# Performance work log

Measured on AMD Instinct MI355X. Metric: run time of the kernel, lower is better.

## Reference

```python
import jax, jax.numpy as jnp
import numpy as np

B_, L_, DM, DS, DC, EX = 4, 2048, 1024, 16, 4, 2
DI = DM * EX

def setup_inputs() -> dict:
    key = jax.random.key(0)
    ks = jax.random.split(key, 8)
    s = lambda i, shape, scale: jax.random.normal(ks[i], shape, jnp.float32) * scale
    return dict(
        x=s(0, (B_, L_, DM), 1.0),
        in_proj_w=s(1, (2 * DI, DM), 0.02),
        conv_weight=s(2, (DI, DC), 0.1),
        conv_bias=jnp.zeros((DI,), jnp.float32),
        A_log=jax.random.uniform(ks[3], (DS,), jnp.float32, -4.0, -1.0),
        D=jnp.ones((DI,), jnp.float32),
        delta_w=s(4, (DS, DI), 0.02),
        delta_b=jnp.ones((DS,), jnp.float32),
        B_w=s(5, (DS, DI), 0.02),
        C_w=s(6, (DS, DI), 0.02),
        out_proj_w=s(7, (DM, DI), 0.02),
    )

def reference(x, in_proj_w, conv_weight, conv_bias, A_log, D, delta_w, delta_b, B_w, C_w, out_proj_w):
    Bb, L, Dm = x.shape
    di, dc = conv_weight.shape
    # 1. input projection and split into ssm / gate branches
    x_inner = x @ in_proj_w.T                       # [B,L,2*di]
    x_ssm, x_gate = x_inner[..., :di], x_inner[..., di:]
    # 2. causal depthwise conv1d + SiLU (kernel size dc, per-channel weights)
    xp = jnp.pad(x_ssm, ((0, 0), (dc - 1, 0), (0, 0)))
    xc = conv_bias + sum(xp[:, k:k + L, :] * conv_weight[:, k] for k in range(dc))
    x_conv = jax.nn.silu(xc)                         # [B,L,di]
    # 3. content-aware discretization
    delta = jax.nn.softplus(x_conv @ delta_w.T + delta_b)  # [B,L,N]
    Bs = x_conv @ B_w.T                              # [B,L,N]
    Cs = x_conv @ C_w.T                              # [B,L,N]
    A = -jnp.exp(A_log)                              # [N]
    xavg = x_conv.mean(axis=-1)                      # [B,L]
    # 4. selective SSM scan over L with state h:[B,N]
    def step(h, inp):
        dt, bt, ct, xa = inp                         # [B,N],[B,N],[B,N],[B]
        h = jnp.exp(dt * A) * h + dt * bt * xa[:, None]
        return h, (h * ct).sum(-1)                   # y_t: [B]
    h0 = jnp.zeros((Bb, A.shape[0]), x.dtype)
    _, ys = jax.lax.scan(
        step, h0,
        (delta.transpose(1, 0, 2), Bs.transpose(1, 0, 2), Cs.transpose(1, 0, 2), xavg.T))
    y_ssm = ys.T[..., None]                          # [B,L,1] (broadcasts over di)
    # 5. gate, skip, output projection
    y_gated = y_ssm * jax.nn.silu(x_gate)
    y_skip = y_gated + x_conv * D
    return y_skip @ out_proj_w.T                     # [B,L,D]
```

## Files before the change

### kernel.cpp

```cpp
#include <hip/hip_runtime.h>
#include <cmath>

#define LL 2048
#define NROW 8192
#define DMODEL 1024
#define DINNER 2048
#define NSTATE 16
#define NSEG 64
#define SEGLEN 32

typedef unsigned short u16;
typedef __attribute__((ext_vector_type(8))) unsigned short u16x8;
typedef __attribute__((ext_vector_type(8))) short short8;
typedef __attribute__((ext_vector_type(4))) float floatx4;
typedef __attribute__((ext_vector_type(16))) float floatx16;

__device__ __forceinline__ float bf2f(u16 h) {
    unsigned u = ((unsigned)h) << 16;
    float f;
    __builtin_memcpy(&f, &u, 4);
    return f;
}
__device__ __forceinline__ u16 f2bf(float f) {
    unsigned u;
    __builtin_memcpy(&u, &f, 4);
    u = u + 0x7fffu + ((u >> 16) & 1u);
    return (u16)(u >> 16);
}
__device__ __forceinline__ float silu_f(float x) { return x / (1.f + __expf(-x)); }

__global__ __launch_bounds__(256) void cvt_multi(
    const float* __restrict__ s0, const float* __restrict__ s1,
    const float* __restrict__ s2, const float* __restrict__ s3,
    const float* __restrict__ s4, const float* __restrict__ s5,
    u16* __restrict__ d0, u16* __restrict__ d1, u16* __restrict__ d2,
    u16* __restrict__ d3, u16* __restrict__ d4, u16* __restrict__ d5) {
    int bid = blockIdx.x;
    const float* s;
    u16* d;
    size_t off;
    if (bid < 4096)      { s = s0; d = d0; off = (size_t)bid * 2048; }
    else if (bid < 6144) { s = s1; d = d1; off = (size_t)(bid - 4096) * 2048; }
    else if (bid < 7168) { s = s2; d = d2; off = (size_t)(bid - 6144) * 2048; }
    else if (bid < 7184) { s = s3; d = d3; off = (size_t)(bid - 7168) * 2048; }
    else if (bid < 7200) { s = s4; d = d4; off = (size_t)(bid - 7184) * 2048; }
    else                 { s = s5; d = d5; off = (size_t)(bid - 7200) * 2048; }
    size_t i = off + (size_t)threadIdx.x * 8;
    float4 a = *(const float4*)&s[i];
    float4 b = *(const float4*)&s[i + 4];
    u16x8 o;
    o[0] = f2bf(a.x); o[1] = f2bf(a.y); o[2] = f2bf(a.z); o[3] = f2bf(a.w);
    o[4] = f2bf(b.x); o[5] = f2bf(b.y); o[6] = f2bf(b.z); o[7] = f2bf(b.w);
    *(u16x8*)&d[i] = o;
}

template <int OUT_BF16>
__global__ __launch_bounds__(256) void gemm_bt_mfma(
    const u16* __restrict__ A, const u16* __restrict__ B,
    void* __restrict__ Cout, int N, int K) {
    __shared__ u16 As[128 * 32];
    __shared__ u16 Bs[128 * 32];
    const int tid = threadIdx.x;
    const int lane = tid & 63;
    const int wave = tid >> 6;
    const int bm = blockIdx.y * 128;
    const int bn = blockIdx.x * 128;

    const int kbg = (lane & 3) ^ ((lane >> 3) & 3);
    const int srow = lane >> 2;
    const u16* ag[2];
    const u16* bg[2];
#pragma unroll
    for (int p = 0; p < 2; ++p) {
        int c = wave * 2 + p;
        ag[p] = A + (size_t)(bm + c * 16 + srow) * K + kbg * 8;
        bg[p] = B + (size_t)(bn + c * 16 + srow) * K + kbg * 8;
    }
    const int frow = lane & 31;
    const int khi = lane >> 5;
    const int wr = (wave >> 1) * 64;
    const int wc = (wave & 1) * 64;
    int aoff[2][2], boff[2][2];
#pragma unroll
    for (int mi = 0; mi < 2; ++mi)
#pragma unroll
        for (int kh = 0; kh < 2; ++kh) {
            int rA = wr + mi * 32 + frow;
            int rB = wc + mi * 32 + frow;
            int kb = kh * 2 + khi;
            aoff[mi][kh] = rA * 32 + (kb ^ ((rA >> 1) & 3)) * 8;
            boff[mi][kh] = rB * 32 + (kb ^ ((rB >> 1) & 3)) * 8;
        }
    floatx16 acc[2][2];
#pragma unroll
    for (int i = 0; i < 2; ++i)
#pragma unroll
        for (int j = 0; j < 2; ++j) acc[i][j] = (floatx16)(0.f);

    for (int k0 = 0; k0 < K; k0 += 32) {
        __syncthreads();
#pragma unroll
        for (int p = 0; p < 2; ++p) {
            int c = wave * 2 + p;
            __builtin_amdgcn_global_load_lds(
                (const __attribute__((address_space(1))) void*)ag[p],
                (__attribute__((address_space(3))) void*)&As[c * 512], 16, 0, 0);
            __builtin_amdgcn_global_load_lds(
                (const __attribute__((address_space(1))) void*)bg[p],
                (__attribute__((address_space(3))) void*)&Bs[c * 512], 16, 0, 0);
            ag[p] += 32;
            bg[p] += 32;
        }
        __syncthreads();
        short8 af[2][2], bf[2][2];
#pragma unroll
        for (int mi = 0; mi < 2; ++mi)
#pragma unroll
            for (int kh = 0; kh < 2; ++kh) {
                af[mi][kh] = *(const short8*)&As[aoff[mi][kh]];
                bf[mi][kh] = *(const short8*)&Bs[boff[mi][kh]];
            }
#pragma unroll
        for (int kh = 0; kh < 2; ++kh)
#pragma unroll
            for (int mi = 0; mi < 2; ++mi)
#pragma unroll
                for (int ni = 0; ni < 2; ++ni)
                    acc[mi][ni] = __builtin_amdgcn_mfma_f32_32x32x16_bf16(
                        af[mi][kh], bf[ni][kh], acc[mi][ni], 0, 0, 0);
    }
    const int cc = lane & 31;
    const int rbase = 4 * (lane >> 5);
#pragma unroll
    for (int mi = 0; mi < 2; ++mi)
#pragma unroll
        for (int ni = 0; ni < 2; ++ni)
#pragma unroll
            for (int r = 0; r < 16; ++r) {
                int grow = bm + wr + mi * 32 + (r & 3) + 8 * (r >> 2) + rbase;
                int gcol = bn + wc + ni * 32 + cc;
                float v = acc[mi][ni][r];
                if (OUT_BF16)
                    ((u16*)Cout)[(size_t)grow * N + gcol] = f2bf(v);
                else
                    ((float*)Cout)[(size_t)grow * N + gcol] = v;
            }
}

__global__ __launch_bounds__(256) void conv_silu_avg(
    const u16* __restrict__ xin, const float* __restrict__ cw,
    const float* __restrict__ cb, u16* __restrict__ xconv,
    float* __restrict__ xavg) {
    const int blk = blockIdx.x;
    const int b = blk >> 7;
    const int lc = blk & 127;
    const int row0 = b * LL + lc * 16;
    const int tid = threadIdx.x;
    const int lane = tid & 63, wave = tid >> 6;
    const int d0 = tid * 8;
    float4 cwv[8];
    float cbv[8];
#pragma unroll
    for (int e = 0; e < 8; ++e) cwv[e] = *(const float4*)&cw[(d0 + e) * 4];
#pragma unroll
    for (int e = 0; e < 8; e += 4) {
        float4 c = *(const float4*)&cb[d0 + e];
        cbv[e] = c.x; cbv[e + 1] = c.y; cbv[e + 2] = c.z; cbv[e + 3] = c.w;
    }
    u16x8 w0, w1, w2;
    if (lc == 0) {
        w0 = (u16x8)0; w1 = (u16x8)0; w2 = (u16x8)0;
    } else {
        w0 = *(const u16x8*)&xin[(size_t)(row0 - 3) * (2 * DINNER) + d0];
        w1 = *(const u16x8*)&xin[(size_t)(row0 - 2) * (2 * DINNER) + d0];
        w2 = *(const u16x8*)&xin[(size_t)(row0 - 1) * (2 * DINNER) + d0];
    }
    float sums[16];
#pragma unroll
    for (int t = 0; t < 16; ++t) {
        u16x8 cur = *(const u16x8*)&xin[(size_t)(row0 + t) * (2 * DINNER) + d0];
        float lsum = 0.f;
        u16x8 o;
#pragma unroll
        for (int e = 0; e < 8; ++e) {
            float acc = cbv[e];
            acc += bf2f(w0[e]) * cwv[e].x;
            acc += bf2f(w1[e]) * cwv[e].y;
            acc += bf2f(w2[e]) * cwv[e].z;
            acc += bf2f(cur[e]) * cwv[e].w;
            float s = silu_f(acc);
            lsum += s;
            o[e] = f2bf(s);
        }
        *(u16x8*)&xconv[(size_t)(row0 + t) * DINNER + d0] = o;
        sums[t] = lsum;
        w0 = w1; w1 = w2; w2 = cur;
    }
#pragma unroll
    for (int off = 32; off; off >>= 1)
#pragma unroll
        for (int t = 0; t < 16; ++t) sums[t] += __shfl_down(sums[t], off);
    __shared__ float wred[4][16];
    if (lane == 0) {
#pragma unroll
        for (int t = 0; t < 16; ++t) wred[wave][t] = sums[t];
    }
    __syncthreads();
    if (tid < 16)
        xavg[row0 + tid] = (wred[0][tid] + wred[1][tid] + wred[2][tid] + wred[3][tid]) *
                           (1.f / DINNER);
}

__global__ __launch_bounds__(256) void dbc_mfma(
    const u16* __restrict__ xconv, const u16* __restrict__ wcat,
    const float* __restrict__ db, const float* __restrict__ A_log,
    const float* __restrict__ xavg,
    float* __restrict__ a_out, float* __restrict__ u_out, float* __restrict__ c_out) {
    __shared__ u16 As[128 * 32];
    __shared__ u16 Bs[48 * 32];
    const int tid = threadIdx.x;
    const int lane = tid & 63;
    const int wave = tid >> 6;
    const int bm = blockIdx.x * 128;

    const int kbg = (lane & 3) ^ ((lane >> 3) & 3);
    const int srow = lane >> 2;
    const u16* ag[2];
#pragma unroll
    for (int p = 0; p < 2; ++p) {
        int c = wave * 2 + p;
        ag[p] = xconv + (size_t)(bm + c * 16 + srow) * DINNER + kbg * 8;
    }
    const u16* bgp = wcat + (size_t)(wave * 16 + srow) * DINNER + kbg * 8;
    const int fr = lane & 15;
    const int kb = lane >> 4;
    const int kbs = kb ^ ((fr >> 1) & 3);
    int aoff[2], boff[3];
#pragma unroll
    for (int mi = 0; mi < 2; ++mi) aoff[mi] = (wave * 32 + mi * 16 + fr) * 32 + kbs * 8;
#pragma unroll
    for (int ni = 0; ni < 3; ++ni) boff[ni] = (ni * 16 + fr) * 32 + kbs * 8;

    floatx4 acc[2][3];
#pragma unroll
    for (int mi = 0; mi < 2; ++mi)
#pragma unroll
        for (int ni = 0; ni < 3; ++ni) acc[mi][ni] = (floatx4){0.f, 0.f, 0.f, 0.f};

    for (int k0 = 0; k0 < DINNER; k0 += 32) {
        __syncthreads();
#pragma unroll
        for (int p = 0; p < 2; ++p) {
            int c = wave * 2 + p;
            __builtin_amdgcn_global_load_lds(
                (const __attribute__((address_space(1))) void*)ag[p],
                (__attribute__((address_space(3))) void*)&As[c * 512], 16, 0, 0);
            ag[p] += 32;
        }
        if (wave < 3) {
            __builtin_amdgcn_global_load_lds(
                (const __attribute__((address_space(1))) void*)bgp,
                (__attribute__((address_space(3))) void*)&Bs[wave * 512], 16, 0, 0);
            bgp += 32;
        }
        __syncthreads();
        short8 af[2], bf[3];
#pragma unroll
        for (int mi = 0; mi < 2; ++mi) af[mi] = *(const short8*)&As[aoff[mi]];
#pragma unroll
        for (int ni = 0; ni < 3; ++ni) bf[ni] = *(const short8*)&Bs[boff[ni]];
#pragma unroll
        for (int mi = 0; mi < 2; ++mi)
#pragma unroll
            for (int ni = 0; ni < 3; ++ni)
                acc[mi][ni] = __builtin_amdgcn_mfma_f32_16x16x32_bf16(af[mi], bf[ni],
                                                                      acc[mi][ni], 0, 0, 0);
    }
    const int cr = (lane >> 4) * 4;
    const int s = lane & 15;
    const float Aa = -__expf(A_log[s]);
    const float dbs = db[s];
#pragma unroll
    for (int mi = 0; mi < 2; ++mi)
#pragma unroll
        for (int r = 0; r < 4; ++r) {
            int row = bm + wave * 32 + mi * 16 + cr + r;
            float pre = acc[mi][0][r] + dbs;
            float delta = (pre > 20.f) ? pre : log1pf(__expf(pre));
            a_out[row * NSTATE + s] = __expf(delta * Aa);
            u_out[row * NSTATE + s] = delta * acc[mi][1][r] * xavg[row];
            c_out[row * NSTATE + s] = acc[mi][2][r];
        }
}

__global__ __launch_bounds__(256) void scan_p1(
    const float* __restrict__ a, const float* __restrict__ u,
    float* __restrict__ Pc, float* __restrict__ H0c) {
    int gid = blockIdx.x * 256 + threadIdx.x;
    int s = gid & 15, seg = (gid >> 4) & (NSEG - 1), b = gid >> 10;
    size_t base = (size_t)(b * LL + seg * SEGLEN) * NSTATE + s;
    float P = 1.f, h = 0.f;
#pragma unroll 8
    for (int t = 0; t < SEGLEN; ++t) {
        float av = a[base + (size_t)t * NSTATE];
        float uv = u[base + (size_t)t * NSTATE];
        h = fmaf(av, h, uv);
        P *= av;
    }
    int o = (b * NSEG + seg) * NSTATE + s;
    Pc[o] = P;
    H0c[o] = h;
}

__global__ __launch_bounds__(64) void scan_p2(
    const float* __restrict__ Pc, const float* __restrict__ H0c,
    float* __restrict__ hstart) {
    int lane = threadIdx.x;
    int b = lane >> 4, s = lane & 15;
    float h = 0.f;
#pragma unroll 8
    for (int seg = 0; seg < NSEG; ++seg) {
        int o = (b * NSEG + seg) * NSTATE + s;
        hstart[o] = h;
        h = fmaf(Pc[o], h, H0c[o]);
    }
}

__global__ __launch_bounds__(256) void scan_p3(
    const float* __restrict__ a, const float* __restrict__ u,
    const float* __restrict__ c, const float* __restrict__ hstart,
    float* __restrict__ y) {
    int gid = blockIdx.x * 256 + threadIdx.x;
    int s = gid & 15, seg = (gid >> 4) & (NSEG - 1), b = gid >> 10;
    float h = hstart[(b * NSEG + seg) * NSTATE + s];
    size_t base = (size_t)(b * LL + seg * SEGLEN) * NSTATE + s;
#pragma unroll 8
    for (int t = 0; t < SEGLEN; ++t) {
        float av = a[base + (size_t)t * NSTATE];
        float uv = u[base + (size_t)t * NSTATE];
        float cv = c[base + (size_t)t * NSTATE];
        h = fmaf(av, h, uv);
        float p = h * cv;
        p += __shfl_xor(p, 1);
        p += __shfl_xor(p, 2);
        p += __shfl_xor(p, 4);
        p += __shfl_xor(p, 8);
        if (s == 0) y[b * LL + seg * SEGLEN + t] = p;
    }
}

__global__ __launch_bounds__(256) void gate_skip(
    const u16* __restrict__ xin, const float* __restrict__ y,
    const float* __restrict__ Dv, const u16* __restrict__ xconv,
    u16* __restrict__ yskip) {
    size_t i = ((size_t)blockIdx.x * 256 + threadIdx.x) * 8;
    int row = (int)(i >> 11);
    int d = (int)(i & (DINNER - 1));
    u16x8 g = *(const u16x8*)&xin[(size_t)row * (2 * DINNER) + DINNER + d];
    u16x8 xc = *(const u16x8*)&xconv[i];
    float yv = y[row];
    u16x8 o;
#pragma unroll
    for (int e = 0; e < 8; ++e) {
        float gv = silu_f(bf2f(g[e]));
        float v = yv * gv + bf2f(xc[e]) * Dv[d + e];
        o[e] = f2bf(v);
    }
    *(u16x8*)&yskip[i] = o;
}

extern "C" void kernel_launch(void* const* d_in, const int* in_sizes, int n_in,
                              void* d_out, int out_size, void* d_ws, size_t ws_size,
                              hipStream_t stream) {
    const float* x       = (const float*)d_in[0];
    const float* w_in    = (const float*)d_in[1];
    const float* conv_w  = (const float*)d_in[2];
    const float* conv_b  = (const float*)d_in[3];
    const float* A_log   = (const float*)d_in[4];
    const float* Dv      = (const float*)d_in[5];
    const float* delta_w = (const float*)d_in[6];
    const float* delta_b = (const float*)d_in[7];
    const float* B_w     = (const float*)d_in[8];
    const float* C_w     = (const float*)d_in[9];
    const float* out_w   = (const float*)d_in[10];
    float* out = (float*)d_out;

    u16* xb  = (u16*)d_ws;
    u16* wb  = xb + 8388608;
    u16* owb = wb + 4194304;
    u16* wsb = owb + 2097152;
    u16* xin = wsb + 98304;
    u16* xcv = xin + 33554432;
    u16* ysk = xcv + 16777216;
    float* fb     = (float*)(ysk + 16777216);
    float* abuf   = fb;
    float* ubuf   = abuf + 131072;
    float* cbuf   = ubuf + 131072;
    float* pbuf   = cbuf + 131072;
    float* h0buf  = pbuf + 4096;
    float* hsbuf  = h0buf + 4096;
    float* ybuf   = hsbuf + 4096;
    float* avgbuf = ybuf + 8192;

    cvt_multi<<<7216, 256, 0, stream>>>(x, w_in, out_w, delta_w, B_w, C_w,
                                        xb, wb, owb, wsb, wsb + 32768, wsb + 65536);

    gemm_bt_mfma<1><<<dim3(32, 64), 256, 0, stream>>>(xb, wb, xin, 2 * DINNER, DMODEL);

    conv_silu_avg<<<512, 256, 0, stream>>>(xin, conv_w, conv_b, xcv, avgbuf);
    dbc_mfma<<<64, 256, 0, stream>>>(xcv, wsb, delta_b, A_log, avgbuf,
                                     abuf, ubuf, cbuf);

    scan_p1<<<16, 256, 0, stream>>>(abuf, ubuf, pbuf, h0buf);
    scan_p2<<<1, 64, 0, stream>>>(pbuf, h0buf, hsbuf);
    scan_p3<<<16, 256, 0, stream>>>(abuf, ubuf, cbuf, hsbuf, ybuf);

    gate_skip<<<NROW * DINNER / 8 / 256, 256, 0, stream>>>(xin, ybuf, Dv, xcv, ysk);

    gemm_bt_mfma<0><<<dim3(8, 64), 256, 0, stream>>>(ysk, owb, out, DMODEL, DINNER);
}
```

Before: 339.5 us.

## Use 256x256-tile, 8-wave double-buffered MFMA GEMM for input projection

Adds a new GEMM kernel for the input projection that uses 256x256 output tiles across 8 waves, where the old kernel used 128x128 tiles across 4 waves. It double-buffers LDS, loads global data straight into LDS with global_load_lds, and interleaves the staging loads with MFMA phases using barriers and s_setprio. The aim is to raise data reuse per byte loaded and to overlap memory traffic with compute on the largest GEMM. In exchange it uses much more LDS and more registers, leaves fewer blocks in the grid (512), and relies on hand-tuned waitcnt counts.

```diff
diff --git a/kernel.cpp b/kernel.cpp
--- a/kernel.cpp
+++ b/kernel.cpp
@@ -55,6 +55,168 @@
 }
 
 template <int OUT_BF16>
+__global__ __launch_bounds__(512, 2) void gemm_bt_256(
+    const u16* __restrict__ A, const u16* __restrict__ B,
+    void* __restrict__ Cout, int N, int K) {
+    __shared__ u16 sA[2][2][256 * 32];
+    __shared__ u16 sB[2][2][256 * 32];
+    const int tid = threadIdx.x;
+    const int lane = tid & 63;
+    const int wave = tid >> 6;
+    const int wm = wave >> 2;
+    const int wn = wave & 3;
+    const int bm = blockIdx.y * 256;
+    const int bn = blockIdx.x * 256;
+
+    const int srow = lane >> 2;
+    const int kbg = (lane & 3) ^ ((lane >> 3) & 3);
+    const u16* aBase[2];
+    const u16* bBase[2];
+#pragma unroll
+    for (int p = 0; p < 2; ++p) {
+        int chunk = wave * 2 + p;
+        aBase[p] = A + (size_t)(bm + chunk * 16 + srow) * K + kbg * 8;
+        bBase[p] = B + (size_t)(bn + chunk * 16 + srow) * K + kbg * 8;
+    }
+    const int ldsOff[2] = {(wave * 2) * 512, (wave * 2 + 1) * 512};
+
+    auto stageA = [&](int buf, int kh, int kt) {
+#pragma unroll
+        for (int p = 0; p < 2; ++p)
+            __builtin_amdgcn_global_load_lds(
+                (const __attribute__((address_space(1))) void*)(aBase[p] + kt * 64 + kh * 32),
+                (__attribute__((address_space(3))) void*)&sA[buf][kh][ldsOff[p]], 16, 0, 0);
+    };
+    auto stageB = [&](int buf, int kh, int kt) {
+#pragma unroll
+        for (int p = 0; p < 2; ++p)
+            __builtin_amdgcn_global_load_lds(
+                (const __attribute__((address_space(1))) void*)(bBase[p] + kt * 64 + kh * 32),
+                (__attribute__((address_space(3))) void*)&sB[buf][kh][ldsOff[p]], 16, 0, 0);
+    };
+
+    const int fr = lane & 15;
+    const int kq = lane >> 4;
+    const int ks2 = kq ^ ((fr >> 1) & 3);
+    int aoff[2][4], boff[4];
+#pragma unroll
+    for (int qm = 0; qm < 2; ++qm)
+#pragma unroll
+        for (int mi = 0; mi < 4; ++mi)
+            aoff[qm][mi] = (wm * 128 + qm * 64 + mi * 16 + fr) * 32 + ks2 * 8;
+#pragma unroll
+    for (int ni = 0; ni < 4; ++ni)
+        boff[ni] = (wn * 64 + ni * 16 + fr) * 32 + ks2 * 8;
+
+    floatx4 acc[8][4];
+#pragma unroll
+    for (int i = 0; i < 8; ++i)
+#pragma unroll
+        for (int j = 0; j < 4; ++j) acc[i][j] = (floatx4){0.f, 0.f, 0.f, 0.f};
+
+    stageA(0, 0, 0);
+    stageB(0, 0, 0);
+    stageA(0, 1, 0);
+    stageB(0, 1, 0);
+    asm volatile("s_waitcnt vmcnt(0)" ::: "memory");
+    __builtin_amdgcn_s_barrier();
+
+    const int NT = K >> 6;
+    for (int t = 0; t < NT; ++t) {
+        const int cur = t & 1;
+        const int nxt = cur ^ 1;
+        int tn = t + 1;
+        if (tn == NT) tn = 0;
+        short8 af[4], bf[4];
+
+#pragma unroll
+        for (int mi = 0; mi < 4; ++mi) af[mi] = *(const short8*)&sA[cur][0][aoff[0][mi]];
+#pragma unroll
+        for (int ni = 0; ni < 4; ++ni) bf[ni] = *(const short8*)&sB[cur][0][boff[ni]];
+        stageA(nxt, 0, tn);
+        __builtin_amdgcn_s_barrier();
+        asm volatile("s_waitcnt lgkmcnt(0)" ::: "memory");
+        __builtin_amdgcn_s_setprio(1);
+#pragma unroll
+        for (int mi = 0; mi < 4; ++mi)
+#pragma unroll
+            for (int ni = 0; ni < 4; ++ni)
+                acc[mi][ni] = __builtin_amdgcn_mfma_f32_16x16x32_bf16(af[mi], bf[ni],
+                                                                      acc[mi][ni], 0, 0, 0);
+        __builtin_amdgcn_s_setprio(0);
+        __builtin_amdgcn_s_barrier();
+
+#pragma unroll
+        for (int mi = 0; mi < 4; ++mi) af[mi] = *(const short8*)&sA[cur][0][aoff[1][mi]];
+        stageB(nxt, 0, tn);
+        __builtin_amdgcn_s_barrier();
+        asm volatile("s_waitcnt lgkmcnt(0)" ::: "memory");
+        __builtin_amdgcn_s_setprio(1);
+#pragma unroll
+        for (int mi = 0; mi < 4; ++mi)
+#pragma unroll
+            for (int ni = 0; ni < 4; ++ni)
+                acc[4 + mi][ni] = __builtin_amdgcn_mfma_f32_16x16x32_bf16(af[mi], bf[ni],
+                                                                          acc[4 + mi][ni], 0, 0, 0);
+        __builtin_amdgcn_s_setprio(0);
+        asm volatile("s_waitcnt vmcnt(4)" ::: "memory");
+        __builtin_amdgcn_s_barrier();
+        __builtin_amdgcn_sched_barrier(0);
+
+#pragma unroll
+        for (int mi = 0; mi < 4; ++mi) af[mi] = *(const short8*)&sA[cur][1][aoff[0][mi]];
+#pragma unroll
+        for (int ni = 0; ni < 4; ++ni) bf[ni] = *(const short8*)&sB[cur][1][boff[ni]];
+        stageA(nxt, 1, tn);
+        __builtin_amdgcn_s_barrier();
+        asm volatile("s_waitcnt lgkmcnt(0)" ::: "memory");
+        __builtin_amdgcn_s_setprio(1);
+#pragma unroll
+        for (int mi = 0; mi < 4; ++mi)
+#pragma unroll
+            for (int ni = 0; ni < 4; ++ni)
+                acc[mi][ni] = __builtin_amdgcn_mfma_f32_16x16x32_bf16(af[mi], bf[ni],
+                                                                      acc[mi][ni], 0, 0, 0);
+        __builtin_amdgcn_s_setprio(0);
+        __builtin_amdgcn_s_barrier();
+
+#pragma unroll
+        for (int mi = 0; mi < 4; ++mi) af[mi] = *(const short8*)&sA[cur][1][aoff[1][mi]];
+        stageB(nxt, 1, tn);
+        __builtin_amdgcn_s_barrier();
+        asm volatile("s_waitcnt lgkmcnt(0)" ::: "memory");
+        __builtin_amdgcn_s_setprio(1);
+#pragma unroll
+        for (int mi = 0; mi < 4; ++mi)
+#pragma unroll
+            for (int ni = 0; ni < 4; ++ni)
+                acc[4 + mi][ni] = __builtin_amdgcn_mfma_f32_16x16x32_bf16(af[mi], bf[ni],
+                                                                          acc[4 + mi][ni], 0, 0, 0);
+        __builtin_amdgcn_s_setprio(0);
+        asm volatile("s_waitcnt vmcnt(4)" ::: "memory");
+        __builtin_amdgcn_s_barrier();
+        __builtin_amdgcn_sched_barrier(0);
+    }
+
+    const int cc = lane & 15;
+    const int rb = (lane >> 4) * 4;
+#pragma unroll
+    for (int mi = 0; mi < 8; ++mi)
+#pragma unroll
+        for (int ni = 0; ni < 4; ++ni)
+#pragma unroll
+            for (int r = 0; r < 4; ++r) {
+                int grow = bm + wm * 128 + mi * 16 + rb + r;
+                int gcol = bn + wn * 64 + ni * 16 + cc;
+                float v = acc[mi][ni][r];
+                if (OUT_BF16)
+                    ((u16*)Cout)[(size_t)grow * N + gcol] = f2bf(v);
+                else
+                    ((float*)Cout)[(size_t)grow * N + gcol] = v;
+            }
+}
+
+template <int OUT_BF16>
 __global__ __launch_bounds__(256) void gemm_bt_mfma(
     const u16* __restrict__ A, const u16* __restrict__ B,
     void* __restrict__ Cout, int N, int K) {
@@ -405,7 +567,7 @@
     cvt_multi<<<7216, 256, 0, stream>>>(x, w_in, out_w, delta_w, B_w, C_w,
                                         xb, wb, owb, wsb, wsb + 32768, wsb + 65536);
 
-    gemm_bt_mfma<1><<<dim3(32, 64), 256, 0, stream>>>(xb, wb, xin, 2 * DINNER, DMODEL);
+    gemm_bt_256<1><<<dim3(16, 32), 512, 0, stream>>>(xb, wb, xin, 2 * DINNER, DMODEL);
 
     conv_silu_avg<<<512, 256, 0, stream>>>(xin, conv_w, conv_b, xcv, avgbuf);
     dbc_mfma<<<64, 256, 0, stream>>>(xcv, wsb, delta_b, A_log, avgbuf,
```

Result: no change. 343.3 us (+1.1%).

## Add 256x256 double-buffered MFMA GEMM for in-proj and split-K dbc kernel

Applied to the files above, without the earlier changes.

The input projection GEMM moves to a new kernel with 256x256 tiles, 8 waves, double-buffered LDS staging via global_load_lds, and explicit waitcnt, barrier and priority scheduling so loads overlap MFMA work. The delta/B/C projection is rewritten to load operands straight from global memory into registers, split K across the four waves and reduce partial sums through LDS, running 256 blocks instead of 64. The goal is more data reuse and latency hiding in the large GEMM and more parallelism in the narrow dbc GEMM. In exchange the GEMM uses 64 KB of LDS per block, which limits occupancy, and its hand-tuned wait counts are fragile.

```diff
diff --git a/kernel.cpp b/kernel.cpp
--- a/kernel.cpp
+++ b/kernel.cpp
@@ -54,6 +54,175 @@
     *(u16x8*)&d[i] = o;
 }
 
+#define GL_LDS(gp, lp)                                                        \
+    __builtin_amdgcn_global_load_lds(                                         \
+        (const __attribute__((address_space(1))) void*)(gp),                  \
+        (__attribute__((address_space(3))) void*)(lp), 16, 0, 0)
+
+template <int OUT_BF16>
+__global__ __launch_bounds__(512, 2) void gemm_bt_256(
+    const u16* __restrict__ A, const u16* __restrict__ B,
+    void* __restrict__ Cout, int N, int K) {
+    __shared__ u16 sA[2][2][256 * 32];
+    __shared__ u16 sB[2][2][256 * 32];
+    const int tid = threadIdx.x;
+    const int lane = tid & 63;
+    const int wave = tid >> 6;
+    const int wm = wave >> 2;
+    const int wn = wave & 3;
+    const int bm = blockIdx.y * 256;
+    const int bn = blockIdx.x * 256;
+
+    const int srow = lane >> 2;
+    const int kbg = (lane & 3) ^ ((lane >> 3) & 3);
+    const u16* aBase[2];
+    const u16* bBase[2];
+#pragma unroll
+    for (int p = 0; p < 2; ++p) {
+        int chunk = wave * 2 + p;
+        aBase[p] = A + (size_t)(bm + chunk * 16 + srow) * K + kbg * 8;
+        bBase[p] = B + (size_t)(bn + chunk * 16 + srow) * K + kbg * 8;
+    }
+    const int ldsOff0 = (wave * 2) * 512;
+    const int ldsOff1 = (wave * 2 + 1) * 512;
+
+#define STAGE_A(buf, kh, kt)                                                  \
+    do {                                                                      \
+        GL_LDS(aBase[0] + (kt) * 64 + (kh) * 32, &sA[buf][kh][ldsOff0]);      \
+        GL_LDS(aBase[1] + (kt) * 64 + (kh) * 32, &sA[buf][kh][ldsOff1]);      \
+    } while (0)
+#define STAGE_B(buf, kh, kt)                                                  \
+    do {                                                                      \
+        GL_LDS(bBase[0] + (kt) * 64 + (kh) * 32, &sB[buf][kh][ldsOff0]);      \
+        GL_LDS(bBase[1] + (kt) * 64 + (kh) * 32, &sB[buf][kh][ldsOff1]);      \
+    } while (0)
+
+    const int fr = lane & 15;
+    const int kq = lane >> 4;
+    const int ks2 = kq ^ ((fr >> 1) & 3);
+    int aoff[2][4], boff[4];
+#pragma unroll
+    for (int qm = 0; qm < 2; ++qm)
+#pragma unroll
+        for (int mi = 0; mi < 4; ++mi)
+            aoff[qm][mi] = (wm * 128 + qm * 64 + mi * 16 + fr) * 32 + ks2 * 8;
+#pragma unroll
+    for (int ni = 0; ni < 4; ++ni)
+        boff[ni] = (wn * 64 + ni * 16 + fr) * 32 + ks2 * 8;
+
+#define READ_A(dst, qm, kh, buf)                                              \
+    do {                                                                      \
+        _Pragma("unroll")                                                     \
+        for (int mi = 0; mi < 4; ++mi)                                        \
+            dst[mi] = *(const short8*)&sA[buf][kh][aoff[qm][mi]];             \
+    } while (0)
+#define READ_B(dst, kh, buf)                                                  \
+    do {                                                                      \
+        _Pragma("unroll")                                                     \
+        for (int ni = 0; ni < 4; ++ni)                                        \
+            dst[ni] = *(const short8*)&sB[buf][kh][boff[ni]];                 \
+    } while (0)
+#define MFMA16(base, AF, BF)                                                  \
+    do {                                                                      \
+        _Pragma("unroll")                                                     \
+        for (int mi = 0; mi < 4; ++mi)                                        \
+            _Pragma("unroll")                                                 \
+            for (int ni = 0; ni < 4; ++ni)                                    \
+                acc[(base) + mi][ni] = __builtin_amdgcn_mfma_f32_16x16x32_bf16( \
+                    AF[mi], BF[ni], acc[(base) + mi][ni], 0, 0, 0);           \
+    } while (0)
+
+    floatx4 acc[8][4];
+#pragma unroll
+    for (int i = 0; i < 8; ++i)
+#pragma unroll
+        for (int j = 0; j < 4; ++j) acc[i][j] = (floatx4){0.f, 0.f, 0.f, 0.f};
+
+    short8 afA[4], afB[4], bfA[4], bfB[4];
+
+    STAGE_A(0, 0, 0);
+    STAGE_B(0, 0, 0);
+    STAGE_A(0, 1, 0);
+    STAGE_B(0, 1, 0);
+    asm volatile("s_waitcnt vmcnt(0)" ::: "memory");
+    __builtin_amdgcn_s_barrier();
+    READ_A(afA, 0, 0, 0);
+    READ_B(bfA, 0, 0);
+    __builtin_amdgcn_sched_barrier(0);
+
+    const int NT = K >> 6;
+    for (int t = 0; t < NT; ++t) {
+        const int cur = t & 1;
+        const int nxt = cur ^ 1;
+        int tn = t + 1;
+        if (tn == NT) tn = 0;
+
+        asm volatile("s_waitcnt lgkmcnt(0)" ::: "memory");
+        __builtin_amdgcn_sched_barrier(0);
+        READ_A(afB, 1, 0, cur);
+        STAGE_A(nxt, 0, tn);
+        __builtin_amdgcn_sched_barrier(0);
+        __builtin_amdgcn_s_setprio(1);
+        MFMA16(0, afA, bfA);
+        __builtin_amdgcn_s_setprio(0);
+
+        asm volatile("s_waitcnt lgkmcnt(0)" ::: "memory");
+        __builtin_amdgcn_sched_barrier(0);
+        asm volatile("s_waitcnt vmcnt(2)" ::: "memory");
+        __builtin_amdgcn_s_barrier();
+        READ_A(afA, 0, 1, cur);
+        READ_B(bfB, 1, cur);
+        STAGE_B(nxt, 0, tn);
+        __builtin_amdgcn_sched_barrier(0);
+        __builtin_amdgcn_s_setprio(1);
+        MFMA16(4, afB, bfA);
+        __builtin_amdgcn_s_setprio(0);
+
+        asm volatile("s_waitcnt lgkmcnt(0)" ::: "memory");
+        __builtin_amdgcn_sched_barrier(0);
+        READ_A(afB, 1, 1, cur);
+        STAGE_A(nxt, 1, tn);
+        __builtin_amdgcn_sched_barrier(0);
+        __builtin_amdgcn_s_setprio(1);
+        MFMA16(0, afA, bfB);
+        __builtin_amdgcn_s_setprio(0);
+
+        asm volatile("s_waitcnt lgkmcnt(0)" ::: "memory");
+        __builtin_amdgcn_sched_barrier(0);
+        asm volatile("s_waitcnt vmcnt(2)" ::: "memory");
+        __builtin_amdgcn_s_barrier();
+        READ_A(afA, 0, 0, nxt);
+        READ_B(bfA, 0, nxt);
+        STAGE_B(nxt, 1, tn);
+        __builtin_amdgcn_sched_barrier(0);
+        __builtin_amdgcn_s_setprio(1);
+        MFMA16(4, afB, bfB);
+        __builtin_amdgcn_s_setprio(0);
+    }
+
+    const int cc = lane & 15;
+    const int rb = (lane >> 4) * 4;
+#pragma unroll
+    for (int mi = 0; mi < 8; ++mi)
+#pragma unroll
+        for (int ni = 0; ni < 4; ++ni)
+#pragma unroll
+            for (int r = 0; r < 4; ++r) {
+                int grow = bm + wm * 128 + mi * 16 + rb + r;
+                int gcol = bn + wn * 64 + ni * 16 + cc;
+                float v = acc[mi][ni][r];
+                if (OUT_BF16)
+                    ((u16*)Cout)[(size_t)grow * N + gcol] = f2bf(v);
+                else
+                    ((float*)Cout)[(size_t)grow * N + gcol] = v;
+            }
+#undef STAGE_A
+#undef STAGE_B
+#undef READ_A
+#undef READ_B
+#undef MFMA16
+}
+
 template <int OUT_BF16>
 __global__ __launch_bounds__(256) void gemm_bt_mfma(
     const u16* __restrict__ A, const u16* __restrict__ B,
@@ -211,35 +380,25 @@
                            (1.f / DINNER);
 }
 
-__global__ __launch_bounds__(256) void dbc_mfma(
+__global__ __launch_bounds__(256) void dbc_direct(
     const u16* __restrict__ xconv, const u16* __restrict__ wcat,
     const float* __restrict__ db, const float* __restrict__ A_log,
     const float* __restrict__ xavg,
     float* __restrict__ a_out, float* __restrict__ u_out, float* __restrict__ c_out) {
-    __shared__ u16 As[128 * 32];
-    __shared__ u16 Bs[48 * 32];
+    __shared__ float part[4][32][48];
     const int tid = threadIdx.x;
     const int lane = tid & 63;
     const int wave = tid >> 6;
-    const int bm = blockIdx.x * 128;
-
-    const int kbg = (lane & 3) ^ ((lane >> 3) & 3);
-    const int srow = lane >> 2;
-    const u16* ag[2];
-#pragma unroll
-    for (int p = 0; p < 2; ++p) {
-        int c = wave * 2 + p;
-        ag[p] = xconv + (size_t)(bm + c * 16 + srow) * DINNER + kbg * 8;
-    }
-    const u16* bgp = wcat + (size_t)(wave * 16 + srow) * DINNER + kbg * 8;
+    const int bm = blockIdx.x * 32;
     const int fr = lane & 15;
-    const int kb = lane >> 4;
-    const int kbs = kb ^ ((fr >> 1) & 3);
-    int aoff[2], boff[3];
-#pragma unroll
-    for (int mi = 0; mi < 2; ++mi) aoff[mi] = (wave * 32 + mi * 16 + fr) * 32 + kbs * 8;
-#pragma unroll
-    for (int ni = 0; ni < 3; ++ni) boff[ni] = (ni * 16 + fr) * 32 + kbs * 8;
+    const int kq = lane >> 4;
+    const int k0 = wave * 512 + kq * 8;
+
+    const u16* ap0 = xconv + (size_t)(bm + fr) * DINNER + k0;
+    const u16* ap1 = xconv + (size_t)(bm + 16 + fr) * DINNER + k0;
+    const u16* bp0 = wcat + (size_t)(fr) * DINNER + k0;
+    const u16* bp1 = wcat + (size_t)(16 + fr) * DINNER + k0;
+    const u16* bp2 = wcat + (size_t)(32 + fr) * DINNER + k0;
 
     floatx4 acc[2][3];
 #pragma unroll
@@ -247,50 +406,49 @@
 #pragma unroll
         for (int ni = 0; ni < 3; ++ni) acc[mi][ni] = (floatx4){0.f, 0.f, 0.f, 0.f};
 
-    for (int k0 = 0; k0 < DINNER; k0 += 32) {
-        __syncthreads();
-#pragma unroll
-        for (int p = 0; p < 2; ++p) {
-            int c = wave * 2 + p;
-            __builtin_amdgcn_global_load_lds(
-                (const __attribute__((address_space(1))) void*)ag[p],
-                (__attribute__((address_space(3))) void*)&As[c * 512], 16, 0, 0);
-            ag[p] += 32;
+#pragma unroll 4
+    for (int kk = 0; kk < 16; ++kk) {
+        short8 a0 = *(const short8*)ap0;
+        short8 a1 = *(const short8*)ap1;
+        short8 b0 = *(const short8*)bp0;
+        short8 b1 = *(const short8*)bp1;
+        short8 b2 = *(const short8*)bp2;
+        ap0 += 32; ap1 += 32; bp0 += 32; bp1 += 32; bp2 += 32;
+        acc[0][0] = __builtin_amdgcn_mfma_f32_16x16x32_bf16(a0, b0, acc[0][0], 0, 0, 0);
+        acc[0][1] = __builtin_amdgcn_mfma_f32_16x16x32_bf16(a0, b1, acc[0][1], 0, 0, 0);
+        acc[0][2] = __builtin_amdgcn_mfma_f32_16x16x32_bf16(a0, b2, acc[0][2], 0, 0, 0);
+        acc[1][0] = __builtin_amdgcn_mfma_f32_16x16x32_bf16(a1, b0, acc[1][0], 0, 0, 0);
+        acc[1][1] = __builtin_amdgcn_mfma_f32_16x16x32_bf16(a1, b1, acc[1][1], 0, 0, 0);
+        acc[1][2] = __builtin_amdgcn_mfma_f32_16x16x32_bf16(a1, b2, acc[1][2], 0, 0, 0);
+    }
+    const int cr = kq * 4;
+#pragma unroll
+    for (int mi = 0; mi < 2; ++mi)
+#pragma unroll
+        for (int ni = 0; ni < 3; ++ni)
+#pragma unroll
+            for (int r = 0; r < 4; ++r)
+                part[wave][mi * 16 + cr + r][ni * 16 + fr] = acc[mi][ni][r];
+    __syncthreads();
+#pragma unroll
+    for (int it = tid; it < 512; it += 256) {
+        int row = it >> 4;
+        int s = it & 15;
+        float sd = 0.f, sb = 0.f, sc = 0.f;
+#pragma unroll
+        for (int w = 0; w < 4; ++w) {
+            sd += part[w][row][s];
+            sb += part[w][row][s + 16];
+            sc += part[w][row][s + 32];
         }
-        if (wave < 3) {
-            __builtin_amdgcn_global_load_lds(
-                (const __attribute__((address_space(1))) void*)bgp,
-                (__attribute__((address_space(3))) void*)&Bs[wave * 512], 16, 0, 0);
-            bgp += 32;
-        }
-        __syncthreads();
-        short8 af[2], bf[3];
-#pragma unroll
-        for (int mi = 0; mi < 2; ++mi) af[mi] = *(const short8*)&As[aoff[mi]];
-#pragma unroll
-        for (int ni = 0; ni < 3; ++ni) bf[ni] = *(const short8*)&Bs[boff[ni]];
-#pragma unroll
-        for (int mi = 0; mi < 2; ++mi)
-#pragma unroll
-            for (int ni = 0; ni < 3; ++ni)
-                acc[mi][ni] = __builtin_amdgcn_mfma_f32_16x16x32_bf16(af[mi], bf[ni],
-                                                                      acc[mi][ni], 0, 0, 0);
-    }
-    const int cr = (lane >> 4) * 4;
-    const int s = lane & 15;
-    const float Aa = -__expf(A_log[s]);
-    const float dbs = db[s];
-#pragma unroll
-    for (int mi = 0; mi < 2; ++mi)
-#pragma unroll
-        for (int r = 0; r < 4; ++r) {
-            int row = bm + wave * 32 + mi * 16 + cr + r;
-            float pre = acc[mi][0][r] + dbs;
-            float delta = (pre > 20.f) ? pre : log1pf(__expf(pre));
-            a_out[row * NSTATE + s] = __expf(delta * Aa);
-            u_out[row * NSTATE + s] = delta * acc[mi][1][r] * xavg[row];
-            c_out[row * NSTATE + s] = acc[mi][2][r];
-        }
+        int grow = bm + row;
+        float Aa = -__expf(A_log[s]);
+        float pre = sd + db[s];
+        float delta = (pre > 20.f) ? pre : log1pf(__expf(pre));
+        a_out[grow * NSTATE + s] = __expf(delta * Aa);
+        u_out[grow * NSTATE + s] = delta * sb * xavg[grow];
+        c_out[grow * NSTATE + s] = sc;
+    }
 }
 
 __global__ __launch_bounds__(256) void scan_p1(
@@ -405,11 +563,11 @@
     cvt_multi<<<7216, 256, 0, stream>>>(x, w_in, out_w, delta_w, B_w, C_w,
                                         xb, wb, owb, wsb, wsb + 32768, wsb + 65536);
 
-    gemm_bt_mfma<1><<<dim3(32, 64), 256, 0, stream>>>(xb, wb, xin, 2 * DINNER, DMODEL);
+    gemm_bt_256<1><<<dim3(16, 32), 512, 0, stream>>>(xb, wb, xin, 2 * DINNER, DMODEL);
 
     conv_silu_avg<<<512, 256, 0, stream>>>(xin, conv_w, conv_b, xcv, avgbuf);
-    dbc_mfma<<<64, 256, 0, stream>>>(xcv, wsb, delta_b, A_log, avgbuf,
-                                     abuf, ubuf, cbuf);
+    dbc_direct<<<256, 256, 0, stream>>>(xcv, wsb, delta_b, A_log, avgbuf,
+                                        abuf, ubuf, cbuf);
 
     scan_p1<<<16, 256, 0, stream>>>(abuf, ubuf, pbuf, h0buf);
     scan_p2<<<1, 64, 0, stream>>>(pbuf, h0buf, hsbuf);
```

Measured after the change: 326.0 us. 1.04x faster.
